# Kernel tuning notes

Measured on AMD Instinct MI355X. Metric: run time of the kernel, lower is better.

Reference implementation:

```python
import jax, jax.numpy as jnp
import numpy as np
from jax import lax

HD = 64      # head_dim
PS = 2       # fine patch size
EPS = 1e-5   # batchnorm eps

def _conv(x, w, stride, pad, groups=1):
    return lax.conv_general_dilated(x, w, (stride, stride), ((pad, pad), (pad, pad)),
                                    feature_group_count=groups,
                                    dimension_numbers=('NCHW', 'OIHW', 'NCHW'))

def _conv_transpose(x, w, stride, pad):
    # torch ConvTranspose2d(in,out,k,stride,pad) with w [in,out,k,k]
    k = w.shape[-1]
    wt = jnp.flip(w, (2, 3)).transpose(1, 0, 2, 3)  # -> [out,in,k,k]
    e = k - 1 - pad
    return lax.conv_general_dilated(x, wt, (1, 1), ((e, e), (e, e)),
                                    lhs_dilation=(stride, stride),
                                    dimension_numbers=('NCHW', 'OIHW', 'NCHW'))

def _bn(x, g, b, m, v):
    inv = g / jnp.sqrt(v + EPS)
    return x * inv[None, :, None, None] + (b - m * inv)[None, :, None, None]

def setup_inputs() -> dict:
    key = jax.random.key(0)
    ks = jax.random.split(key, 12)
    B, C, H, W = 8, 256, 64, 64
    f = lambda k, sh, s=0.05: jax.random.normal(k, sh, jnp.float32) * s
    return {
        'x': jax.random.normal(ks[0], (B, C, H, W), jnp.float32),
        'down_w': f(ks[1], (C, C, 4, 4), 0.02), 'down_b': f(ks[2], (C,)),
        'up_w': f(ks[3], (C, C, 4, 4), 0.02), 'up_b': f(ks[4], (C,)),
        'wqkv_c': f(ks[5], (HD, 3 * HD)), 'bqkv_c': f(ks[6], (3 * HD,)),
        'wqkv_f': f(ks[7], (HD, 3 * HD)), 'bqkv_f': f(ks[8], (3 * HD,)),
        'dw_w': f(ks[9], (C, 1, 3, 3)),
        'bn1_g': jnp.ones((C,), jnp.float32), 'bn1_b': jnp.zeros((C,), jnp.float32),
        'bn1_m': jnp.zeros((C,), jnp.float32), 'bn1_v': jnp.ones((C,), jnp.float32),
        'pw_w': f(ks[10], (C, C, 1, 1)),
        'bn2_g': jnp.ones((C,), jnp.float32), 'bn2_b': jnp.zeros((C,), jnp.float32),
        'bn2_m': jnp.zeros((C,), jnp.float32), 'bn2_v': jnp.ones((C,), jnp.float32),
    }

def reference(x, down_w, down_b, up_w, up_b, wqkv_c, bqkv_c, wqkv_f, bqkv_f, dw_w,
              bn1_g, bn1_b, bn1_m, bn1_v, pw_w, bn2_g, bn2_b, bn2_m, bn2_v):
    B, C, H, W = x.shape
    nh = C // HD
    scale = HD ** -0.5

    # ---- CoarseSelfAttention: downsample -> per-head MHSA -> top-k -> upsample ----
    xd = _conv(x, down_w, 2, 1) + down_b[None, :, None, None]          # [B,C,H/2,W/2]
    h, w = H // 2, W // 2
    N = h * w
    tok = xd.reshape(B, nh, HD, N).transpose(0, 1, 3, 2)               # [B,nh,N,hd]
    q, k, v = jnp.split(tok @ wqkv_c + bqkv_c, 3, axis=-1)
    attn = jax.nn.softmax(jnp.einsum('bhnd,bhmd->bhnm', q, k) * scale, axis=-1)
    score = attn.sum(axis=-2)                                          # [B,nh,N]
    kf = max(1, N // 4)
    topk = lax.top_k(score, kf)[1]                                     # [B,nh,kf] int32
    out = jnp.einsum('bhnm,bhmd->bhnd', attn, v)
    out = out.transpose(0, 1, 3, 2).reshape(B, C, h, w)
    coarse = _conv_transpose(out, up_w, 2, 1) + up_b[None, :, None, None]  # [B,C,H,W]
    # F.interpolate to (H,W) is identity here: upsample output already matches x.

    # ---- TopkSelfAttention: gather top-k 2x2 patches, local MHSA, scatter back ----
    ph, pw = H // PS, W // PS
    xh = coarse.reshape(B, nh, HD, ph, PS, pw, PS)
    patches = xh.transpose(0, 1, 2, 3, 5, 4, 6).reshape(B, nh, HD, ph * pw, PS, PS)
    sel = jnp.take_along_axis(patches, topk[:, :, None, :, None, None], axis=3)  # [B,nh,hd,kf,PS,PS]
    tok_f = sel.reshape(B, nh, HD, kf, PS * PS).transpose(0, 1, 3, 4, 2).reshape(B, nh, kf * PS * PS, HD)
    qf, kfp, vf = jnp.split(tok_f @ wqkv_f + bqkv_f, 3, axis=-1)
    attn_f = jax.nn.softmax(jnp.einsum('bhnd,bhmd->bhnm', qf, kfp) * scale, axis=-1)
    out_f = jnp.einsum('bhnm,bhmd->bhnd', attn_f, vf)                  # [B,nh,kf*4,hd]
    out_p = out_f.reshape(B, nh, kf, PS * PS, HD).transpose(0, 1, 2, 4, 3).reshape(B, nh, kf, HD, PS, PS)
    bi = jnp.arange(B)[:, None, None]
    hi = jnp.arange(nh)[None, :, None]
    res = jnp.zeros_like(patches).at[bi, hi, :, topk].set(out_p)       # scatter (indices unique)
    region = res.reshape(B, nh, HD, ph, pw, PS, PS).transpose(0, 1, 2, 3, 5, 4, 6).reshape(B, C, H, W)

    # ---- residual + DWConv (depthwise->BN->ReLU6->pointwise->BN->ReLU6) ----
    y = coarse + region
    y = jnp.clip(_bn(_conv(y, dw_w, 1, 1, groups=C), bn1_g, bn1_b, bn1_m, bn1_v), 0.0, 6.0)
    y = jnp.clip(_bn(_conv(y, pw_w, 1, 0), bn2_g, bn2_b, bn2_m, bn2_v), 0.0, 6.0)
    return y
```

## Files before the change

### kernel.cpp

```cpp
#include <hip/hip_runtime.h>
#include <hip/hip_bf16.h>

typedef __hip_bfloat16 bf16;
typedef __bf16 bf16x8 __attribute__((ext_vector_type(8)));
typedef float f32x4 __attribute__((ext_vector_type(4)));


#define OFF_XDHWC    0L
#define OFF_QH       2097152L
#define OFF_T1       0L
#define OFF_OUTC     8388608L
#define OFF_COARSE   10485760L
#define OFF_XHL      10485760L
#define OFF_PSCW     10485760L
#define OFF_SCORE    19398656L
#define OFF_TOPK     19431424L
#define OFF_DOWNW    19439616L
#define OFF_DOWNWL   19963904L
#define OFF_UPW4     20488192L
#define OFF_WQKVC    21536768L
#define OFF_BQKVC    21549056L
#define OFF_WQKVF    21549248L
#define OFF_BQKVF    21561536L
#define OFF_PWW      21561728L
#define OFF_DWW      21627264L
#define OFF_BN1S     21629568L
#define OFF_BN1T     21629824L
#define OFF_BN2S     21630080L
#define OFF_BN2T     21630336L
#define OFF_DOWNB    21630592L
#define OFF_UPB      21630848L
#define OFF_FLAG     21631104L
#define WS_FLOATS    21631360L

__device__ __forceinline__ float relu6(float v) { return v < 0.f ? 0.f : (v > 6.f ? 6.f : v); }

__device__ __forceinline__ float ldin(const void* p, long i, int flag) {
    return flag ? __bfloat162float(((const bf16*)p)[i]) : ((const float*)p)[i];
}

__device__ __forceinline__ unsigned short f2bf(float f) {
    unsigned int b = __float_as_uint(f);
    b += 0x7FFFu + ((b >> 16) & 1u);
    return (unsigned short)(b >> 16);
}

__global__ __launch_bounds__(256) void detect_kernel(const void* __restrict__ x, int* __restrict__ flag) {
    __shared__ int cnt[256];
    int tid = threadIdx.x;
    int c = 0;
    for (int i = tid; i < 4096; i += 256) {
        long idx = (long)i * 2047;
        float v = __bfloat162float(((const bf16*)x)[idx]);
        float a = fabsf(v);
        if (isfinite(v) && a > 1e-8f && a < 100.f) c++;
    }
    cnt[tid] = c; __syncthreads();
    for (int s = 128; s > 0; s >>= 1) { if (tid < s) cnt[tid] += cnt[tid + s]; __syncthreads(); }
    if (tid == 0 && cnt[0] >= 3686) *flag = 1;
}

__global__ __launch_bounds__(256) void cvt_kernel(const void* __restrict__ in, float* __restrict__ out,
                                                  int n, const int* __restrict__ flagp) {
    int flag = *flagp;
    int i = blockIdx.x * 256 + threadIdx.x;
    if (i < n) out[i] = ldin(in, i, flag);
}

__global__ __launch_bounds__(256) void cvt_bf16_kernel(const void* __restrict__ in, unsigned short* __restrict__ out,
                                                       int n, const int* __restrict__ flagp) {
    int flag = *flagp;
    int i = blockIdx.x * 256 + threadIdx.x;
    if (i < n) out[i] = f2bf(ldin(in, i, flag));
}

__global__ __launch_bounds__(256) void split_pack_kernel(const void* __restrict__ in, unsigned int* __restrict__ out,
                                                         int n, const int* __restrict__ flagp) {
    int flag = *flagp;
    int i = blockIdx.x * 256 + threadIdx.x;
    if (i < n) {
        float v = ldin(in, i, flag);
        unsigned short h = f2bf(v);
        float fh = __uint_as_float(((unsigned int)h) << 16);
        unsigned short l = f2bf(v - fh);
        out[i] = (unsigned int)h | ((unsigned int)l << 16);
    }
}

__global__ __launch_bounds__(256) void split_kernel(const void* __restrict__ in,
                                                    unsigned short* __restrict__ hi, unsigned short* __restrict__ lo,
                                                    int n, const int* __restrict__ flagp) {
    int flag = *flagp;
    int i = blockIdx.x * 256 + threadIdx.x;
    if (i < n) {
        float v = ldin(in, i, flag);
        unsigned short h = f2bf(v);
        float fh = __uint_as_float(((unsigned int)h) << 16);
        hi[i] = h;
        lo[i] = f2bf(v - fh);
    }
}

__global__ __launch_bounds__(256) void tqkv_kernel(const void* __restrict__ w, float* __restrict__ wt,
                                                   const int* __restrict__ flagp) {
    int flag = *flagp;
    int idx = blockIdx.x * 256 + threadIdx.x;
    if (idx >= 192 * 64) return;
    int j = idx >> 6, d = idx & 63;
    wt[idx] = ldin(w, d * 192 + j, flag);
}

__global__ __launch_bounds__(256) void prep_up_kernel(const void* __restrict__ w, unsigned short* __restrict__ W4,
                                                      const int* __restrict__ flagp) {
    int flag = *flagp;
    int idx = blockIdx.x * 256 + threadIdx.x;
    int cls = idx >> 18; int rem = idx & 262143;
    int co = rem >> 10; int q = rem & 1023;
    int ci = q >> 2; int j = q & 3;
    int pa = cls >> 1, pb = cls & 1;
    int jy = j >> 1, jx = j & 1;
    int ky = (pa == 0) ? (jy ? 3 : 1) : (jy ? 0 : 2);
    int kx = (pb == 0) ? (jx ? 3 : 1) : (jx ? 0 : 2);
    W4[idx] = f2bf(ldin(w, (((long)ci * 256 + co) * 4 + ky) * 4 + kx, flag));
}

__global__ void bn_prep_kernel(const void* __restrict__ g, const void* __restrict__ b,
                               const void* __restrict__ m, const void* __restrict__ v,
                               float* __restrict__ s, float* __restrict__ t,
                               const int* __restrict__ flagp) {
    int flag = *flagp;
    int c = threadIdx.x;
    float gv = ldin(g, c, flag), bv = ldin(b, c, flag);
    float mv = ldin(m, c, flag), vv = ldin(v, c, flag);
    float inv = gv / sqrtf(vv + 1e-5f);
    s[c] = inv; t[c] = bv - mv * inv;
}

__global__ __launch_bounds__(256) void gemm_mfma_x2(
    const unsigned int* __restrict__ XHL,
    const unsigned short* __restrict__ WH, const unsigned short* __restrict__ WL,
    float* __restrict__ C, const float* __restrict__ e0)
{
    __shared__ __align__(16) unsigned short Ah[64 * 40];
    __shared__ __align__(16) unsigned short Al[64 * 40];
    __shared__ __align__(16) unsigned short Bh[64 * 40];
    __shared__ __align__(16) unsigned short Bl[64 * 40];
    int m0 = blockIdx.y * 64, n0 = blockIdx.x * 64;
    int tid = threadIdx.x;
    int w = tid >> 6, l = tid & 63, l15 = l & 15, q = l >> 4;
    unsigned int aR[8];
    uint4 bhR, blR;
    int bn = tid >> 2, bk = (tid & 3) * 8;

    auto loadA = [&](int k0) {
        #pragma unroll
        for (int i = 0; i < 8; i++) {
            int idx = i * 256 + tid;
            int kl = idx & 31, ml = idx >> 5;
            int m = m0 + ml, k = k0 + kl;
            int b = m >> 10, oy = (m >> 5) & 31, ox = m & 31;
            int c = k >> 4, ky = (k >> 2) & 3, kx = k & 3;
            int iy = 2 * oy - 1 + ky, ix = 2 * ox - 1 + kx;
            unsigned int v = 0;
            if ((unsigned)iy < 64u && (unsigned)ix < 64u)
                v = XHL[(((long)b * 256 + c) * 64 + iy) * 64 + ix];
            aR[i] = v;
        }
    };
    auto storeA = [&]() {
        #pragma unroll
        for (int i = 0; i < 8; i++) {
            int idx = i * 256 + tid;
            int kl = idx & 31, ml = idx >> 5;
            Ah[ml * 40 + kl] = (unsigned short)(aR[i] & 0xffffu);
            Al[ml * 40 + kl] = (unsigned short)(aR[i] >> 16);
        }
    };
    auto loadB = [&](int k0) {
        bhR = *(const uint4*)(WH + (long)(n0 + bn) * 4096 + (k0 + bk));
        blR = *(const uint4*)(WL + (long)(n0 + bn) * 4096 + (k0 + bk));
    };

    f32x4 acc[4] = {};
    loadA(0); loadB(0);
    for (int k0 = 0; k0 < 4096; k0 += 32) {
        storeA();
        *(uint4*)(&Bh[bn * 40 + bk]) = bhR;
        *(uint4*)(&Bl[bn * 40 + bk]) = blR;
        __syncthreads();
        if (k0 + 32 < 4096) { loadA(k0 + 32); loadB(k0 + 32); }
        bf16x8 afh = *(const bf16x8*)(&Ah[(w * 16 + l15) * 40 + q * 8]);
        bf16x8 afl = *(const bf16x8*)(&Al[(w * 16 + l15) * 40 + q * 8]);
        #pragma unroll
        for (int j4 = 0; j4 < 4; j4++) {
            bf16x8 bfh = *(const bf16x8*)(&Bh[(j4 * 16 + l15) * 40 + q * 8]);
            bf16x8 bfl = *(const bf16x8*)(&Bl[(j4 * 16 + l15) * 40 + q * 8]);
            acc[j4] = __builtin_amdgcn_mfma_f32_16x16x32_bf16(afh, bfh, acc[j4], 0, 0, 0);
            acc[j4] = __builtin_amdgcn_mfma_f32_16x16x32_bf16(afh, bfl, acc[j4], 0, 0, 0);
            acc[j4] = __builtin_amdgcn_mfma_f32_16x16x32_bf16(afl, bfh, acc[j4], 0, 0, 0);
        }
        __syncthreads();
    }
    #pragma unroll
    for (int j4 = 0; j4 < 4; j4++) {
        int n = n0 + j4 * 16 + l15;
        #pragma unroll
        for (int r = 0; r < 4; r++) {
            int m = m0 + w * 16 + q * 4 + r;
            C[(long)m * 256 + n] = acc[j4][r] + e0[n];
        }
    }
}

template<int EPI>
__global__ __launch_bounds__(256) void gemm_k(
    const float* __restrict__ A, const float* __restrict__ B, unsigned short* __restrict__ out,
    int K, int sAm, int sBn, const float* __restrict__ e0)
{
    __shared__ float As[16][68];
    __shared__ float Bs[16][68];
    int m0 = blockIdx.y * 64;
    int n0 = blockIdx.x * 64;
    int tid = threadIdx.x;
    int tx = tid & 15, ty = tid >> 4;
    int l4 = tid >> 2, kq = (tid & 3) * 4;
    float4 aR, bR;

    auto loadA = [&](int k0) { aR = *(const float4*)(A + (long)(m0 + l4) * sAm + (k0 + kq)); };
    auto loadB = [&](int k0) { bR = *(const float4*)(B + (long)(n0 + l4) * sBn + (k0 + kq)); };

    float acc[4][4] = {};
    loadA(0); loadB(0);
    for (int k0 = 0; k0 < K; k0 += 16) {
        As[kq + 0][l4] = aR.x; As[kq + 1][l4] = aR.y; As[kq + 2][l4] = aR.z; As[kq + 3][l4] = aR.w;
        Bs[kq + 0][l4] = bR.x; Bs[kq + 1][l4] = bR.y; Bs[kq + 2][l4] = bR.z; Bs[kq + 3][l4] = bR.w;
        __syncthreads();
        if (k0 + 16 < K) { loadA(k0 + 16); loadB(k0 + 16); }
        #pragma unroll
        for (int kk = 0; kk < 16; ++kk) {
            float4 av = *reinterpret_cast<const float4*>(&As[kk][ty * 4]);
            float4 bv = *reinterpret_cast<const float4*>(&Bs[kk][tx * 4]);
            float a[4] = {av.x, av.y, av.z, av.w};
            float b[4] = {bv.x, bv.y, bv.z, bv.w};
            #pragma unroll
            for (int i = 0; i < 4; i++)
                #pragma unroll
                for (int j = 0; j < 4; j++)
                    acc[i][j] += a[i] * b[j];
        }
        __syncthreads();
    }
    #pragma unroll
    for (int i = 0; i < 4; i++) {
        int m = m0 + ty * 4 + i;
        int bh, tok;
        if (EPI == 2) { int bi = m >> 12; int h = m & 3; tok = (m >> 2) & 1023; bh = bi * 4 + h; }
        else          { bh = m >> 10; tok = m & 1023; }
        #pragma unroll
        for (int j = 0; j < 4; j++) {
            int n = n0 + tx * 4 + j;
            float v = acc[i][j] + e0[n];
            if (n < 64) {
                v *= 0.125f;
                unsigned short hb = f2bf(v);
                float fh = __uint_as_float(((unsigned int)hb) << 16);
                unsigned short lb = f2bf(v - fh);
                long p = (((long)bh << 10) + tok) * 64 + n;
                out[p] = hb; out[p + 2097152] = lb;
            } else if (n < 128) {
                unsigned short hb = f2bf(v);
                float fh = __uint_as_float(((unsigned int)hb) << 16);
                unsigned short lb = f2bf(v - fh);
                long p = (((long)bh << 10) + tok) * 64 + (n - 64);
                out[p + 4194304] = hb; out[p + 6291456] = lb;
            } else {
                out[8388608 + (((long)bh << 6) + (n - 128)) * 1024 + tok] = f2bf(v);
            }
        }
    }
}

template<int EPI, int AMODE>
__global__ __launch_bounds__(256) void gemm_mfma(
    const float* __restrict__ A, const unsigned short* __restrict__ Bb, float* __restrict__ C,
    int K, long sAz, long sBz, int sAk, int sBn,
    const float* __restrict__ e0, const float* __restrict__ e1,
    void* __restrict__ ob, const int* __restrict__ flagp)
{
    __shared__ __align__(16) unsigned short Asb[64 * 40];
    __shared__ __align__(16) unsigned short Bsb[64 * 40];
    int z = blockIdx.z;
    if (AMODE == 0) A += (long)z * sAz;
    Bb += (long)z * sBz;
    int m0 = blockIdx.y * 64, n0 = blockIdx.x * 64;
    int tid = threadIdx.x;
    int w = tid >> 6, l = tid & 63;
    int l15 = l & 15, q = l >> 4;
    float aR[8];
    uint4 bR;

    auto loadA = [&](int k0) {
        if (AMODE == 0) {
            #pragma unroll
            for (int i = 0; i < 8; i++) {
                int idx = i * 256 + tid;
                int ml = idx & 63, kl = idx >> 6;
                aR[i] = A[(long)(k0 + kl) * sAk + (m0 + ml)];
            }
        } else {
            #pragma unroll
            for (int i = 0; i < 8; i++) {
                int idx = i * 256 + tid;
                int kl = idx & 31, ml = idx >> 5;
                int m = m0 + ml, k = k0 + kl;
                int b = m >> 10, y = (m >> 5) & 31, x2 = m & 31;
                int ci = k >> 2, j = k & 3;
                int pa = z >> 1, pb = z & 1;
                int jy = j >> 1, jx = j & 1;
                int dy = (pa == 0) ? (jy ? -1 : 0) : (jy ? 1 : 0);
                int dx = (pb == 0) ? (jx ? -1 : 0) : (jx ? 1 : 0);
                int yy = y + dy, xx = x2 + dx;
                float val = 0.f;
                if ((unsigned)yy < 32u && (unsigned)xx < 32u)
                    val = A[(((long)b * 4 + (ci >> 6)) * 1024 + yy * 32 + xx) * 64 + (ci & 63)];
                aR[i] = val;
            }
        }
    };
    auto storeA = [&]() {
        #pragma unroll
        for (int i = 0; i < 8; i++) {
            int idx = i * 256 + tid;
            int ml, kl;
            if (AMODE == 0) { ml = idx & 63; kl = idx >> 6; }
            else            { kl = idx & 31; ml = idx >> 5; }
            Asb[ml * 40 + kl] = f2bf(aR[i]);
        }
    };
    int bn = tid >> 2, bk = (tid & 3) * 8;
    auto loadB = [&](int k0) {
        bR = *(const uint4*)(Bb + (long)(n0 + bn) * sBn + (k0 + bk));
    };

    f32x4 acc[4] = {};
    loadA(0); loadB(0);
    for (int k0 = 0; k0 < K; k0 += 32) {
        storeA();
        *(uint4*)(&Bsb[bn * 40 + bk]) = bR;
        __syncthreads();
        if (k0 + 32 < K) { loadA(k0 + 32); loadB(k0 + 32); }
        bf16x8 af = *(const bf16x8*)(&Asb[(w * 16 + l15) * 40 + q * 8]);
        #pragma unroll
        for (int j4 = 0; j4 < 4; j4++) {
            bf16x8 bf = *(const bf16x8*)(&Bsb[(j4 * 16 + l15) * 40 + q * 8]);
            acc[j4] = __builtin_amdgcn_mfma_f32_16x16x32_bf16(af, bf, acc[j4], 0, 0, 0);
        }
        __syncthreads();
    }
    int oflag = (EPI == 5) ? *flagp : 0;
    #pragma unroll
    for (int j4 = 0; j4 < 4; j4++) {
        int n = n0 + j4 * 16 + l15;
        #pragma unroll
        for (int r = 0; r < 4; r++) {
            int m = m0 + w * 16 + q * 4 + r;
            float v = acc[j4][r];
            if (EPI == 4) {
                v += e0[n];
                int pa = z >> 1, pb = z & 1;
                int bi = m >> 10, y = (m >> 5) & 31, x2 = m & 31;
                C[(((long)bi * 256 + n) * 64 + (2 * y + pa)) * 64 + (2 * x2 + pb)] = v;
            } else {
                v = relu6(v * e0[n] + e1[n]);
                long oidx = (long)z * 1048576 + (long)n * 4096 + m;
                if (oflag) ((bf16*)ob)[oidx] = __float2bfloat16(v);
                else       ((float*)ob)[oidx] = v;
            }
        }
    }
}

template<bool SCORE>
__global__ __launch_bounds__(256) void attn_mfma(
    const unsigned short* __restrict__ P0,
    float* __restrict__ O, float* __restrict__ PSCW)
{
    const unsigned short* QH = P0;
    const unsigned short* QL = P0 + 2097152;
    const unsigned short* KH = P0 + 4194304;
    const unsigned short* KL = P0 + 6291456;
    const unsigned short* VT = P0 + 8388608;
    __shared__ __align__(16) unsigned short Khs[64 * 72];
    __shared__ __align__(16) unsigned short Kls[64 * 72];
    __shared__ __align__(16) unsigned short Vs[64 * 72];
    __shared__ __align__(16) unsigned short Ps[4][16 * 72];
    int bh = blockIdx.y, rt = blockIdx.x;
    int tid = threadIdx.x;
    int w = tid >> 6, l = tid & 63, l15 = l & 15, q = l >> 4;

    long qoff = (((long)bh << 10) + rt * 64 + w * 16 + l15) * 64 + q * 8;
    bf16x8 afh[2], afl[2];
    afh[0] = *(const bf16x8*)(QH + qoff);
    afh[1] = *(const bf16x8*)(QH + qoff + 32);
    afl[0] = *(const bf16x8*)(QL + qoff);
    afl[1] = *(const bf16x8*)(QL + qoff + 32);

    float mr[4], lr[4];
    #pragma unroll
    for (int r = 0; r < 4; r++) { mr[r] = -1e30f; lr[r] = 0.f; }
    f32x4 o[4] = {};

    auto stageK = [&](int t) {
        #pragma unroll
        for (int i = 0; i < 2; i++) {
            int u = tid + i * 256;
            int tok = u >> 3, dp = (u & 7) * 8;
            long g = (((long)bh << 10) + t * 64 + tok) * 64 + dp;
            *(uint4*)(Khs + tok * 72 + dp) = *(const uint4*)(KH + g);
            *(uint4*)(Kls + tok * 72 + dp) = *(const uint4*)(KL + g);
        }
    };
    auto stageV = [&](int t) {
        #pragma unroll
        for (int i = 0; i < 2; i++) {
            int u = tid + i * 256;
            int d = u >> 3, k0 = (u & 7) * 8;
            long g = (((long)bh << 6) + d) * 1024 + t * 64 + k0;
            *(uint4*)(Vs + d * 72 + k0) = *(const uint4*)(VT + g);
        }
    };
    auto computeS = [&](f32x4* s) {
        #pragma unroll
        for (int kk = 0; kk < 2; kk++)
            #pragma unroll
            for (int j4 = 0; j4 < 4; j4++) {
                bf16x8 kh8 = *(const bf16x8*)(&Khs[(j4 * 16 + l15) * 72 + kk * 32 + q * 8]);
                bf16x8 kl8 = *(const bf16x8*)(&Kls[(j4 * 16 + l15) * 72 + kk * 32 + q * 8]);
                s[j4] = __builtin_amdgcn_mfma_f32_16x16x32_bf16(afh[kk], kh8, s[j4], 0, 0, 0);
                s[j4] = __builtin_amdgcn_mfma_f32_16x16x32_bf16(afh[kk], kl8, s[j4], 0, 0, 0);
                s[j4] = __builtin_amdgcn_mfma_f32_16x16x32_bf16(afl[kk], kh8, s[j4], 0, 0, 0);
            }
    };
    auto pv = [&]() {
        #pragma unroll
        for (int kk = 0; kk < 2; kk++) {
            bf16x8 ap = *(const bf16x8*)(&Ps[w][l15 * 72 + kk * 32 + q * 8]);
            #pragma unroll
            for (int j4 = 0; j4 < 4; j4++) {
                bf16x8 bv = *(const bf16x8*)(&Vs[(j4 * 16 + l15) * 72 + kk * 32 + q * 8]);
                o[j4] = __builtin_amdgcn_mfma_f32_16x16x32_bf16(ap, bv, o[j4], 0, 0, 0);
            }
        }
    };

    if (SCORE) {
        for (int t = 0; t < 16; ++t) {
            __syncthreads();
            stageK(t);
            __syncthreads();
            f32x4 s[4] = {};
            computeS(s);
            #pragma unroll
            for (int r = 0; r < 4; r++) {
                float tm = fmaxf(fmaxf(s[0][r], s[1][r]), fmaxf(s[2][r], s[3][r]));
                #pragma unroll
                for (int off = 1; off < 16; off <<= 1) tm = fmaxf(tm, __shfl_xor(tm, off));
                float mn = fmaxf(mr[r], tm);
                float ss = __expf(s[0][r] - mn) + __expf(s[1][r] - mn)
                         + __expf(s[2][r] - mn) + __expf(s[3][r] - mn);
                #pragma unroll
                for (int off = 1; off < 16; off <<= 1) ss += __shfl_xor(ss, off);
                lr[r] = lr[r] * __expf(mr[r] - mn) + ss;
                mr[r] = mn;
            }
        }
        float linv[4];
        #pragma unroll
        for (int r = 0; r < 4; r++) linv[r] = 1.f / lr[r];
        for (int t = 0; t < 16; ++t) {
            __syncthreads();
            stageK(t); stageV(t);
            __syncthreads();
            f32x4 s[4] = {};
            computeS(s);
            float cs[4] = {0.f, 0.f, 0.f, 0.f};
            #pragma unroll
            for (int j4 = 0; j4 < 4; j4++)
                #pragma unroll
                for (int r = 0; r < 4; r++) {
                    float p = __expf(s[j4][r] - mr[r]) * linv[r];
                    cs[j4] += p;
                    Ps[w][(q * 4 + r) * 72 + j4 * 16 + l15] = f2bf(p);
                }
            #pragma unroll
            for (int j4 = 0; j4 < 4; j4++) {
                cs[j4] += __shfl_xor(cs[j4], 16);
                cs[j4] += __shfl_xor(cs[j4], 32);
            }
            if (q == 0) {
                long pb = (((long)(bh * 16 + rt) * 4 + w) << 10) + t * 64;
                #pragma unroll
                for (int j4 = 0; j4 < 4; j4++) PSCW[pb + j4 * 16 + l15] = cs[j4];
            }
            __syncthreads();
            pv();
        }
    } else {
        for (int t = 0; t < 16; ++t) {
            __syncthreads();
            stageK(t); stageV(t);
            __syncthreads();
            f32x4 s[4] = {};
            computeS(s);
            float corr[4];
            #pragma unroll
            for (int r = 0; r < 4; r++) {
                float tm = fmaxf(fmaxf(s[0][r], s[1][r]), fmaxf(s[2][r], s[3][r]));
                #pragma unroll
                for (int off = 1; off < 16; off <<= 1) tm = fmaxf(tm, __shfl_xor(tm, off));
                float mn = fmaxf(mr[r], tm);
                corr[r] = __expf(mr[r] - mn);
                mr[r] = mn;
            }
            float ssr[4] = {0.f, 0.f, 0.f, 0.f};
            #pragma unroll
            for (int j4 = 0; j4 < 4; j4++)
                #pragma unroll
                for (int r = 0; r < 4; r++) {
                    float p = __expf(s[j4][r] - mr[r]);
                    ssr[r] += p;
                    Ps[w][(q * 4 + r) * 72 + j4 * 16 + l15] = f2bf(p);
                }
            #pragma unroll
            for (int r = 0; r < 4; r++) {
                float ss = ssr[r];
                #pragma unroll
                for (int off = 1; off < 16; off <<= 1) ss += __shfl_xor(ss, off);
                lr[r] = lr[r] * corr[r] + ss;
            }
            #pragma unroll
            for (int j4 = 0; j4 < 4; j4++)
                #pragma unroll
                for (int r = 0; r < 4; r++) o[j4][r] *= corr[r];
            __syncthreads();
            pv();
        }
    }

    float fin[4];
    #pragma unroll
    for (int r = 0; r < 4; r++) fin[r] = SCORE ? 1.f : (1.f / lr[r]);
    long obase = (((long)bh << 10) + rt * 64 + w * 16 + q * 4) * 64;
    #pragma unroll
    for (int j4 = 0; j4 < 4; j4++)
        #pragma unroll
        for (int r = 0; r < 4; r++)
            O[obase + (long)r * 64 + j4 * 16 + l15] = o[j4][r] * fin[r];
}

__global__ __launch_bounds__(256) void score_reduce_kernel(const float* __restrict__ PSCW, float* __restrict__ score) {
    int idx = blockIdx.x * 256 + threadIdx.x;
    int bh = idx >> 10, c = idx & 1023;
    float s = 0.f;
    for (int rw = 0; rw < 64; rw++) s += PSCW[(((long)bh * 64 + rw) << 10) + c];
    score[idx] = s;
}

__global__ __launch_bounds__(256) void topk_kernel(const float* __restrict__ score, int* __restrict__ topk) {
    __shared__ float s[1024];
    int z = blockIdx.x; int tid = threadIdx.x;
    for (int i = tid; i < 1024; i += 256) {
        float v = score[z * 1024 + i];
        s[i] = (v == v) ? v : -INFINITY;
    }
    __syncthreads();
    for (int i = tid; i < 1024; i += 256) {
        float si = s[i]; int r = 0;
        for (int j = 0; j < 1024; j++) {
            float sj = s[j];
            r += (sj > si) || (sj == si && j < i);
        }
        if (r < 256) topk[z * 256 + r] = i;
    }
}

__global__ __launch_bounds__(256) void gather_tokf_kernel(const float* __restrict__ coarse,
                                                          const int* __restrict__ topk,
                                                          float* __restrict__ tokf) {
    long idx = (long)blockIdx.x * 256 + threadIdx.x;
    int d = (int)(idx & 63); int t = (int)((idx >> 6) & 3);
    int j = (int)((idx >> 8) & 255); int bh = (int)(idx >> 16);
    int p = topk[bh * 256 + j] & 1023;
    int py = p >> 5, px = p & 31;
    int dy = t >> 1, dx = t & 1;
    int b = bh >> 2, h = bh & 3;
    tokf[idx] = coarse[(((long)b * 256 + h * 64 + d) * 64 + (2 * py + dy)) * 64 + (2 * px + dx)];
}

__global__ __launch_bounds__(256) void scatter_add_kernel(float* __restrict__ coarse,
                                                          const int* __restrict__ topk,
                                                          const float* __restrict__ outf) {
    long idx = (long)blockIdx.x * 256 + threadIdx.x;
    int d = (int)(idx & 63); int t = (int)((idx >> 6) & 3);
    int j = (int)((idx >> 8) & 255); int bh = (int)(idx >> 16);
    int p = topk[bh * 256 + j] & 1023;
    int py = p >> 5, px = p & 31;
    int dy = t >> 1, dx = t & 1;
    int b = bh >> 2, h = bh & 3;
    coarse[(((long)b * 256 + h * 64 + d) * 64 + (2 * py + dy)) * 64 + (2 * px + dx)] += outf[idx];
}

__global__ __launch_bounds__(64) void dw_bn_relu6_kernel(const float* __restrict__ y, const float* __restrict__ w9,
                                                         const float* __restrict__ s1, const float* __restrict__ t1,
                                                         float* __restrict__ out) {
    int gid = blockIdx.x;
    int row = gid & 63; int bc = gid >> 6; int c = bc & 255;
    int x = threadIdx.x;
    const float* base = y + (long)bc * 4096;
    float acc = 0.f;
    #pragma unroll
    for (int ky = 0; ky < 3; ky++) {
        int yy = row + ky - 1;
        if (yy < 0 || yy >= 64) continue;
        #pragma unroll
        for (int kx = 0; kx < 3; kx++) {
            int xx = x + kx - 1;
            if (xx < 0 || xx >= 64) continue;
            acc += base[yy * 64 + xx] * w9[c * 9 + ky * 3 + kx];
        }
    }
    out[(long)gid * 64 + x] = relu6(acc * s1[c] + t1[c]);
}

extern "C" void kernel_launch(void* const* d_in, const int* in_sizes, int n_in,
                              void* d_out, int out_size, void* d_ws, size_t ws_size,
                              hipStream_t stream) {
    if (ws_size < (size_t)WS_FLOATS * 4) return;

    const void* x      = d_in[0];
    const void* down_w = d_in[1];
    const void* down_b = d_in[2];
    const void* up_w   = d_in[3];
    const void* up_b   = d_in[4];
    const void* wqkv_c = d_in[5];
    const void* bqkv_c = d_in[6];
    const void* wqkv_f = d_in[7];
    const void* bqkv_f = d_in[8];
    const void* dw_w   = d_in[9];
    const void* bn1_g  = d_in[10];
    const void* bn1_b  = d_in[11];
    const void* bn1_m  = d_in[12];
    const void* bn1_v  = d_in[13];
    const void* pw_w   = d_in[14];
    const void* bn2_g  = d_in[15];
    const void* bn2_b  = d_in[16];
    const void* bn2_m  = d_in[17];
    const void* bn2_v  = d_in[18];

    float* ws = (float*)d_ws;
    int* flagp = (int*)(ws + OFF_FLAG);
    dim3 blk(256);

    hipMemsetAsync(flagp, 0, sizeof(int), stream);
    detect_kernel<<<1, blk, 0, stream>>>(x, flagp);

    split_pack_kernel<<<32768, blk, 0, stream>>>(x, (unsigned int*)(ws + OFF_XHL), 8388608, flagp);
    split_kernel<<<4096, blk, 0, stream>>>(down_w, (unsigned short*)(ws + OFF_DOWNW),
                                           (unsigned short*)(ws + OFF_DOWNWL), 1048576, flagp);
    cvt_kernel<<<1, blk, 0, stream>>>(down_b, ws + OFF_DOWNB, 256, flagp);
    cvt_kernel<<<1, blk, 0, stream>>>(up_b, ws + OFF_UPB, 256, flagp);
    cvt_kernel<<<1, blk, 0, stream>>>(bqkv_c, ws + OFF_BQKVC, 192, flagp);
    cvt_kernel<<<1, blk, 0, stream>>>(bqkv_f, ws + OFF_BQKVF, 192, flagp);
    cvt_bf16_kernel<<<256, blk, 0, stream>>>(pw_w, (unsigned short*)(ws + OFF_PWW), 65536, flagp);
    cvt_kernel<<<9, blk, 0, stream>>>(dw_w, ws + OFF_DWW, 2304, flagp);
    tqkv_kernel<<<48, blk, 0, stream>>>(wqkv_c, ws + OFF_WQKVC, flagp);
    tqkv_kernel<<<48, blk, 0, stream>>>(wqkv_f, ws + OFF_WQKVF, flagp);
    prep_up_kernel<<<4096, blk, 0, stream>>>(up_w, (unsigned short*)(ws + OFF_UPW4), flagp);
    bn_prep_kernel<<<1, blk, 0, stream>>>(bn1_g, bn1_b, bn1_m, bn1_v, ws + OFF_BN1S, ws + OFF_BN1T, flagp);
    bn_prep_kernel<<<1, blk, 0, stream>>>(bn2_g, bn2_b, bn2_m, bn2_v, ws + OFF_BN2S, ws + OFF_BN2T, flagp);

    gemm_mfma_x2<<<dim3(4, 128, 1), blk, 0, stream>>>((const unsigned int*)(ws + OFF_XHL),
        (const unsigned short*)(ws + OFF_DOWNW), (const unsigned short*)(ws + OFF_DOWNWL),
        ws + OFF_XDHWC, ws + OFF_DOWNB);

    gemm_k<2><<<dim3(3, 512, 1), blk, 0, stream>>>(ws + OFF_XDHWC, ws + OFF_WQKVC,
        (unsigned short*)(ws + OFF_QH), 64, 64, 64, ws + OFF_BQKVC);

    attn_mfma<true><<<dim3(16, 32), blk, 0, stream>>>((const unsigned short*)(ws + OFF_QH),
        ws + OFF_OUTC, ws + OFF_PSCW);
    score_reduce_kernel<<<128, blk, 0, stream>>>(ws + OFF_PSCW, ws + OFF_SCORE);
    topk_kernel<<<32, blk, 0, stream>>>(ws + OFF_SCORE, (int*)(ws + OFF_TOPK));

    gemm_mfma<4, 2><<<dim3(4, 128, 4), blk, 0, stream>>>(ws + OFF_OUTC, (unsigned short*)(ws + OFF_UPW4),
        ws + OFF_COARSE, 1024, 0, 262144, 0, 1024, ws + OFF_UPB, nullptr, nullptr, flagp);

    gather_tokf_kernel<<<8192, blk, 0, stream>>>(ws + OFF_COARSE, (const int*)(ws + OFF_TOPK), ws + OFF_XDHWC);
    gemm_k<3><<<dim3(3, 512, 1), blk, 0, stream>>>(ws + OFF_XDHWC, ws + OFF_WQKVF,
        (unsigned short*)(ws + OFF_QH), 64, 64, 64, ws + OFF_BQKVF);
    attn_mfma<false><<<dim3(16, 32), blk, 0, stream>>>((const unsigned short*)(ws + OFF_QH),
        ws + OFF_OUTC, nullptr);
    scatter_add_kernel<<<8192, blk, 0, stream>>>(ws + OFF_COARSE, (const int*)(ws + OFF_TOPK), ws + OFF_OUTC);

    dw_bn_relu6_kernel<<<131072, dim3(64), 0, stream>>>(ws + OFF_COARSE, ws + OFF_DWW,
        ws + OFF_BN1S, ws + OFF_BN1T, ws + OFF_T1);

    gemm_mfma<5, 0><<<dim3(4, 64, 8), blk, 0, stream>>>(ws + OFF_T1, (unsigned short*)(ws + OFF_PWW),
        nullptr, 256, 1048576, 0, 4096, 256, ws + OFF_BN2S, ws + OFF_BN2T, d_out, flagp);
}
```

Before: 797.4 us.

## Stage raw input rows in LDS for downsample conv GEMM instead of im2col

Reworks the stride-2 4x4 downsample convolution GEMM. Each block now covers 128 output pixels (four output rows) and K=64 (four channels) per step. Instead of gathering im2col elements one by one, it loads the contiguous packed hi/lo input rows (10 rows x 66 columns per channel) into shared memory once, using precomputed offsets. It then builds the MFMA A-fragments directly from LDS with byte permutes that split the high and low bf16 halves. This is meant to cut redundant global gathers and per-element index arithmetic and to raise MFMA work per barrier, at the cost of more registers and a grid with half as many blocks.

```diff
diff --git a/kernel.cpp b/kernel.cpp
--- a/kernel.cpp
+++ b/kernel.cpp
@@ -4,6 +4,7 @@
 typedef __hip_bfloat16 bf16;
 typedef __bf16 bf16x8 __attribute__((ext_vector_type(8)));
 typedef float f32x4 __attribute__((ext_vector_type(4)));
+typedef unsigned int uintx4 __attribute__((ext_vector_type(4)));
 
 
 #define OFF_XDHWC    0L
@@ -141,75 +142,111 @@
     const unsigned short* __restrict__ WH, const unsigned short* __restrict__ WL,
     float* __restrict__ C, const float* __restrict__ e0)
 {
-    __shared__ __align__(16) unsigned short Ah[64 * 40];
-    __shared__ __align__(16) unsigned short Al[64 * 40];
-    __shared__ __align__(16) unsigned short Bh[64 * 40];
-    __shared__ __align__(16) unsigned short Bl[64 * 40];
-    int m0 = blockIdx.y * 64, n0 = blockIdx.x * 64;
+    __shared__ __align__(16) unsigned int Xs[40 * 68];
+    __shared__ __align__(16) unsigned short Bh[64 * 72];
+    __shared__ __align__(16) unsigned short Bl[64 * 72];
+    int m0 = blockIdx.y * 128, n0 = blockIdx.x * 64;
     int tid = threadIdx.x;
     int w = tid >> 6, l = tid & 63, l15 = l & 15, q = l >> 4;
-    unsigned int aR[8];
-    uint4 bhR, blR;
-    int bn = tid >> 2, bk = (tid & 3) * 8;
+
+    int offA[11], ldsA[11];
+    {
+        int b = m0 >> 10;
+        int iy0 = ((m0 >> 5) & 31) * 2 - 1;
+        #pragma unroll
+        for (int s = 0; s < 11; s++) {
+            int u = s * 256 + tid;
+            offA[s] = -1; ldsA[s] = -1;
+            if (u < 2640) {
+                int R = u / 66;
+                int col = u - R * 66;
+                int cl = R / 10;
+                int rowl = R - cl * 10;
+                ldsA[s] = R * 68 + col;
+                int iy = iy0 + rowl, ix = col - 1;
+                if ((unsigned)iy < 64u && (unsigned)ix < 64u)
+                    offA[s] = ((b * 256 + cl) * 64 + iy) * 64 + ix;
+            }
+        }
+    }
+    unsigned int aR[11];
+    uint4 bhR[2], blR[2];
+    int bn = tid >> 2, bkc = (tid & 3) * 16;
 
     auto loadA = [&](int k0) {
-        #pragma unroll
-        for (int i = 0; i < 8; i++) {
-            int idx = i * 256 + tid;
-            int kl = idx & 31, ml = idx >> 5;
-            int m = m0 + ml, k = k0 + kl;
-            int b = m >> 10, oy = (m >> 5) & 31, ox = m & 31;
-            int c = k >> 4, ky = (k >> 2) & 3, kx = k & 3;
-            int iy = 2 * oy - 1 + ky, ix = 2 * ox - 1 + kx;
-            unsigned int v = 0;
-            if ((unsigned)iy < 64u && (unsigned)ix < 64u)
-                v = XHL[(((long)b * 256 + c) * 64 + iy) * 64 + ix];
-            aR[i] = v;
-        }
+        int cb = (k0 >> 4) * 4096;
+        #pragma unroll
+        for (int s = 0; s < 11; s++)
+            aR[s] = (offA[s] >= 0) ? XHL[offA[s] + cb] : 0u;
     };
     auto storeA = [&]() {
         #pragma unroll
-        for (int i = 0; i < 8; i++) {
-            int idx = i * 256 + tid;
-            int kl = idx & 31, ml = idx >> 5;
-            Ah[ml * 40 + kl] = (unsigned short)(aR[i] & 0xffffu);
-            Al[ml * 40 + kl] = (unsigned short)(aR[i] >> 16);
-        }
+        for (int s = 0; s < 11; s++)
+            if (ldsA[s] >= 0) Xs[ldsA[s]] = aR[s];
     };
     auto loadB = [&](int k0) {
-        bhR = *(const uint4*)(WH + (long)(n0 + bn) * 4096 + (k0 + bk));
-        blR = *(const uint4*)(WL + (long)(n0 + bn) * 4096 + (k0 + bk));
-    };
-
-    f32x4 acc[4] = {};
+        const unsigned short* ph = WH + (long)(n0 + bn) * 4096 + k0 + bkc;
+        const unsigned short* pl = WL + (long)(n0 + bn) * 4096 + k0 + bkc;
+        bhR[0] = *(const uint4*)(ph); bhR[1] = *(const uint4*)(ph + 8);
+        blR[0] = *(const uint4*)(pl); blR[1] = *(const uint4*)(pl + 8);
+    };
+    auto storeB = [&]() {
+        *(uint4*)(&Bh[bn * 72 + bkc]) = bhR[0]; *(uint4*)(&Bh[bn * 72 + bkc + 8]) = bhR[1];
+        *(uint4*)(&Bl[bn * 72 + bkc]) = blR[0]; *(uint4*)(&Bl[bn * 72 + bkc + 8]) = blR[1];
+    };
+
+    f32x4 acc[2][4] = {};
     loadA(0); loadB(0);
-    for (int k0 = 0; k0 < 4096; k0 += 32) {
-        storeA();
-        *(uint4*)(&Bh[bn * 40 + bk]) = bhR;
-        *(uint4*)(&Bl[bn * 40 + bk]) = blR;
+    for (int k0 = 0; k0 < 4096; k0 += 64) {
+        storeA(); storeB();
         __syncthreads();
-        if (k0 + 32 < 4096) { loadA(k0 + 32); loadB(k0 + 32); }
-        bf16x8 afh = *(const bf16x8*)(&Ah[(w * 16 + l15) * 40 + q * 8]);
-        bf16x8 afl = *(const bf16x8*)(&Al[(w * 16 + l15) * 40 + q * 8]);
+        if (k0 + 64 < 4096) { loadA(k0 + 64); loadB(k0 + 64); }
+        #pragma unroll
+        for (int kk = 0; kk < 2; kk++) {
+            bf16x8 bh4[4], bl4[4];
+            #pragma unroll
+            for (int j4 = 0; j4 < 4; j4++) {
+                bh4[j4] = *(const bf16x8*)(&Bh[(j4 * 16 + l15) * 72 + kk * 32 + q * 8]);
+                bl4[j4] = *(const bf16x8*)(&Bl[(j4 * 16 + l15) * 72 + kk * 32 + q * 8]);
+            }
+            int R0 = (kk * 2 + (q >> 1)) * 10 + 2 * w + 2 * (q & 1);
+            #pragma unroll
+            for (int ms = 0; ms < 2; ms++) {
+                const unsigned int* rp = &Xs[R0 * 68 + 2 * (ms * 16 + l15)];
+                uint2 p01 = *(const uint2*)(rp);
+                uint2 p23 = *(const uint2*)(rp + 2);
+                uint2 p45 = *(const uint2*)(rp + 68);
+                uint2 p67 = *(const uint2*)(rp + 70);
+                union { uintx4 u; bf16x8 v; } uh, ul;
+                uh.u[0] = __builtin_amdgcn_perm(p01.y, p01.x, 0x05040100u);
+                ul.u[0] = __builtin_amdgcn_perm(p01.y, p01.x, 0x07060302u);
+                uh.u[1] = __builtin_amdgcn_perm(p23.y, p23.x, 0x05040100u);
+                ul.u[1] = __builtin_amdgcn_perm(p23.y, p23.x, 0x07060302u);
+                uh.u[2] = __builtin_amdgcn_perm(p45.y, p45.x, 0x05040100u);
+                ul.u[2] = __builtin_amdgcn_perm(p45.y, p45.x, 0x07060302u);
+                uh.u[3] = __builtin_amdgcn_perm(p67.y, p67.x, 0x05040100u);
+                ul.u[3] = __builtin_amdgcn_perm(p67.y, p67.x, 0x07060302u);
+                #pragma unroll
+                for (int j4 = 0; j4 < 4; j4++) {
+                    acc[ms][j4] = __builtin_amdgcn_mfma_f32_16x16x32_bf16(uh.v, bh4[j4], acc[ms][j4], 0, 0, 0);
+                    acc[ms][j4] = __builtin_amdgcn_mfma_f32_16x16x32_bf16(uh.v, bl4[j4], acc[ms][j4], 0, 0, 0);
+                    acc[ms][j4] = __builtin_amdgcn_mfma_f32_16x16x32_bf16(ul.v, bh4[j4], acc[ms][j4], 0, 0, 0);
+                }
+            }
+        }
+        __syncthreads();
+    }
+    #pragma unroll
+    for (int ms = 0; ms < 2; ms++)
         #pragma unroll
         for (int j4 = 0; j4 < 4; j4++) {
-            bf16x8 bfh = *(const bf16x8*)(&Bh[(j4 * 16 + l15) * 40 + q * 8]);
-            bf16x8 bfl = *(const bf16x8*)(&Bl[(j4 * 16 + l15) * 40 + q * 8]);
-            acc[j4] = __builtin_amdgcn_mfma_f32_16x16x32_bf16(afh, bfh, acc[j4], 0, 0, 0);
-            acc[j4] = __builtin_amdgcn_mfma_f32_16x16x32_bf16(afh, bfl, acc[j4], 0, 0, 0);
-            acc[j4] = __builtin_amdgcn_mfma_f32_16x16x32_bf16(afl, bfh, acc[j4], 0, 0, 0);
-        }
-        __syncthreads();
-    }
-    #pragma unroll
-    for (int j4 = 0; j4 < 4; j4++) {
-        int n = n0 + j4 * 16 + l15;
-        #pragma unroll
-        for (int r = 0; r < 4; r++) {
-            int m = m0 + w * 16 + q * 4 + r;
-            C[(long)m * 256 + n] = acc[j4][r] + e0[n];
-        }
-    }
+            int n = n0 + j4 * 16 + l15;
+            #pragma unroll
+            for (int r = 0; r < 4; r++) {
+                int m = m0 + w * 32 + ms * 16 + q * 4 + r;
+                C[(long)m * 256 + n] = acc[ms][j4][r] + e0[n];
+            }
+        }
 }
 
 template<int EPI>
@@ -679,7 +716,7 @@
     bn_prep_kernel<<<1, blk, 0, stream>>>(bn1_g, bn1_b, bn1_m, bn1_v, ws + OFF_BN1S, ws + OFF_BN1T, flagp);
     bn_prep_kernel<<<1, blk, 0, stream>>>(bn2_g, bn2_b, bn2_m, bn2_v, ws + OFF_BN2S, ws + OFF_BN2T, flagp);
 
-    gemm_mfma_x2<<<dim3(4, 128, 1), blk, 0, stream>>>((const unsigned int*)(ws + OFF_XHL),
+    gemm_mfma_x2<<<dim3(4, 64, 1), blk, 0, stream>>>((const unsigned int*)(ws + OFF_XHL),
         (const unsigned short*)(ws + OFF_DOWNW), (const unsigned short*)(ws + OFF_DOWNWL),
         ws + OFF_XDHWC, ws + OFF_DOWNB);
 
```

Result: slower. 850.7 us (+6.7%).
